# Kernel tuning notes

Hardware: AMD Instinct MI355X
Metric: run time of the kernel (lower is better)

## Reference

```python
import jax, jax.numpy as jnp
import numpy as np

B, I, D = 2048, 4096, 512          # batch of candidates, num rated items, item_dim
IE, UE = 512, 1024                 # item_emb, user_emb
D1, D2, D3 = 1024, 512, 256        # MLP dense widths


def setup_inputs() -> dict:
    key = jax.random.key(0)
    ks = jax.random.split(key, 16)
    s = 0.02  # weight init scale
    candidate_items = jax.random.normal(ks[0], (B, D), dtype=jnp.float32)
    rated_items = jax.random.normal(ks[1], (I, D), dtype=jnp.float32)
    ratings = jax.random.uniform(ks[2], (B, I), dtype=jnp.float32, minval=0.5, maxval=5.0)
    keep = jax.random.uniform(ks[3], (B, I)) < 0.05
    user_matrix = jnp.where(keep, ratings, 0.0)
    return dict(
        candidate_items=candidate_items,
        rated_items=rated_items,
        user_matrix=user_matrix,
        att_w=jax.random.normal(ks[4], (2 * D, 1), dtype=jnp.float32) * s,
        att_b=jnp.zeros((1,), jnp.float32),
        iw1=jax.random.normal(ks[5], (D, 2 * IE), dtype=jnp.float32) * s,
        ib1=jnp.zeros((2 * IE,), jnp.float32),
        iw2=jax.random.normal(ks[6], (2 * IE, IE), dtype=jnp.float32) * s,
        ib2=jnp.zeros((IE,), jnp.float32),
        uw1=jax.random.normal(ks[7], (D, 2 * UE), dtype=jnp.float32) * s,
        ub1=jnp.zeros((2 * UE,), jnp.float32),
        uw2=jax.random.normal(ks[8], (2 * UE, UE), dtype=jnp.float32) * s,
        ub2=jnp.zeros((UE,), jnp.float32),
        mw1=jax.random.normal(ks[9], (IE + UE, D1), dtype=jnp.float32) * s,
        mb1=jnp.zeros((D1,), jnp.float32),
        mw2=jax.random.normal(ks[10], (D1, D2), dtype=jnp.float32) * s,
        mb2=jnp.zeros((D2,), jnp.float32),
        mw3=jax.random.normal(ks[11], (D2, D3), dtype=jnp.float32) * s,
        mb3=jnp.zeros((D3,), jnp.float32),
        mw4=jax.random.normal(ks[12], (D3, 1), dtype=jnp.float32) * s,
        mb4=jnp.zeros((1,), jnp.float32),
    )


def reference(candidate_items, rated_items, user_matrix,
              att_w, att_b, iw1, ib1, iw2, ib2, uw1, ub1, uw2, ub2,
              mw1, mb1, mw2, mb2, mw3, mb3, mw4, mb4):
    d = candidate_items.shape[1]
    # AttentionNet(Linear(2D,1)) on cat(cand_repeat, rated_tile) decomposes exactly:
    # score[b,i] = cand[b] @ w_c + rated[i] @ w_r + b  (same math, no (B*I,2D) blowup)
    wc, wr = att_w[:d], att_w[d:]                      # (D,1), (D,1)
    scores = candidate_items @ wc + (rated_items @ wr).T + att_b  # (B, I)
    scores = jnp.where(user_matrix == 0.0, -jnp.inf, scores)
    att = jax.nn.softmax(scores, axis=1)
    att = jnp.nan_to_num(att, nan=0.0, posinf=0.0, neginf=0.0)  # rows with no ratings -> 0
    user_feat = (att * user_matrix) @ rated_items      # (B, D)
    # dual towers (dropout = identity in eval)
    item_emb = jax.nn.relu(jax.nn.relu(candidate_items @ iw1 + ib1) @ iw2 + ib2)
    user_emb = jax.nn.relu(jax.nn.relu(user_feat @ uw1 + ub1) @ uw2 + ub2)
    x = jnp.concatenate([item_emb, user_emb], axis=1)  # (B, IE+UE)
    x = jax.nn.relu(x @ mw1 + mb1)
    x = jax.nn.relu(x @ mw2 + mb2)
    x = jax.nn.relu(x @ mw3 + mb3)
    return x @ mw4 + mb4                               # (B, 1)
```

## Files before the change

### kernel.cpp

```cpp
#include <hip/hip_runtime.h>
#include <cstddef>

constexpr int Bn = 2048;
constexpr int In = 4096;
constexpr int Dn = 512;

typedef _Float16 f16;
typedef _Float16 f16x8 __attribute__((ext_vector_type(8)));
typedef _Float16 f16x4 __attribute__((ext_vector_type(4)));
typedef float    f32x4 __attribute__((ext_vector_type(4)));

__global__ __launch_bounds__(256) void k_rs(const float* __restrict__ rated,
                                            const float* __restrict__ att_w,
                                            float* __restrict__ rs) {
  const int wid  = threadIdx.x >> 6;
  const int lane = threadIdx.x & 63;
  const int i = blockIdx.x * 4 + wid;
  const float* row = rated + (size_t)i * Dn;
  const float* wr  = att_w + Dn;
  float s = 0.f;
  #pragma unroll
  for (int d = 0; d < Dn / 64; ++d)
    s = fmaf(row[lane + d * 64], wr[lane + d * 64], s);
  #pragma unroll
  for (int off = 32; off > 0; off >>= 1) s += __shfl_down(s, off);
  if (lane == 0) rs[i] = s;
}

__global__ __launch_bounds__(256) void k_userfeat(const float* __restrict__ um,
                                                  const float* __restrict__ rs,
                                                  const float* __restrict__ rated,
                                                  f16* __restrict__ uf) {
  __shared__ unsigned short s_idx[In];
  __shared__ float s_coef[In];
  __shared__ float s_red[8];
  __shared__ int s_cnt;
  const int tid = threadIdx.x;
  const int b = blockIdx.x;
  if (tid == 0) s_cnt = 0;
  __syncthreads();

  const float* umrow = um + (size_t)b * In;
  float lmax = -INFINITY;
  #pragma unroll
  for (int it = 0; it < In / 256; ++it) {
    const int i = tid + it * 256;
    const float u = umrow[i];
    if (u != 0.0f) {
      const int p = atomicAdd(&s_cnt, 1);
      s_idx[p] = (unsigned short)i;
      s_coef[p] = u;
      lmax = fmaxf(lmax, rs[i]);
    }
  }
  __syncthreads();
  const int n = s_cnt;

  #pragma unroll
  for (int off = 32; off > 0; off >>= 1) lmax = fmaxf(lmax, __shfl_down(lmax, off));
  if ((tid & 63) == 0) s_red[tid >> 6] = lmax;
  __syncthreads();
  const float m = fmaxf(fmaxf(s_red[0], s_red[1]), fmaxf(s_red[2], s_red[3]));
  __syncthreads();

  float lsum = 0.f;
  for (int j = tid; j < n; j += 256) {
    const float t = __expf(rs[s_idx[j]] - m);
    lsum += t;
    s_coef[j] = t * s_coef[j];
  }
  __syncthreads();
  #pragma unroll
  for (int off = 32; off > 0; off >>= 1) lsum += __shfl_down(lsum, off);
  if ((tid & 63) == 0) s_red[tid >> 6] = lsum;
  __syncthreads();
  const float S = s_red[0] + s_red[1] + s_red[2] + s_red[3];
  const float inv = (n > 0 && S > 0.f) ? 1.0f / S : 0.0f;

  float a0 = 0.f, a1 = 0.f;
  for (int j = 0; j < n; ++j) {
    const float c = s_coef[j];
    const float* rrow = rated + (size_t)s_idx[j] * Dn;
    a0 = fmaf(c, rrow[tid], a0);
    a1 = fmaf(c, rrow[tid + 256], a1);
  }
  uf[(size_t)b * Dn + tid]       = (f16)(a0 * inv);
  uf[(size_t)b * Dn + tid + 256] = (f16)(a1 * inv);
}

__global__ __launch_bounds__(256) void k_transpose_f2h(const float* __restrict__ src,
                                                       f16* __restrict__ dst,
                                                       int K, int N) {
  __shared__ float tile[32][33];
  const int tx = threadIdx.x & 31;
  const int ty = threadIdx.x >> 5;
  const int n0 = blockIdx.x * 32;
  const int k0 = blockIdx.y * 32;
  #pragma unroll
  for (int i = 0; i < 4; ++i)
    tile[ty + i * 8][tx] = src[(size_t)(k0 + ty + i * 8) * N + n0 + tx];
  __syncthreads();
  #pragma unroll
  for (int i = 0; i < 4; ++i)
    dst[(size_t)(n0 + ty + i * 8) * K + k0 + tx] = (f16)tile[tx][ty + i * 8];
}

__global__ __launch_bounds__(256) void k_cast_f2h(const float* __restrict__ src,
                                                  f16* __restrict__ dst, int n) {
  const int i = (blockIdx.x * 256 + threadIdx.x) * 4;
  if (i < n) {
    const float4 v = *reinterpret_cast<const float4*>(src + i);
    f16x4 h; h.x = (f16)v.x; h.y = (f16)v.y; h.z = (f16)v.z; h.w = (f16)v.w;
    *reinterpret_cast<f16x4*>(dst + i) = h;
  }
}

template <bool RELU>
__global__ __launch_bounds__(256) void k_hgemm(const f16* __restrict__ A,
                                               const f16* __restrict__ Wt,
                                               const float* __restrict__ bias,
                                               f16* __restrict__ C, int ldc,
                                               int N, int K) {
  __shared__ __align__(16) f16 As[64][40];
  __shared__ __align__(16) f16 Bs[64][40];

  const int tid  = threadIdx.x;
  const int lane = tid & 63;
  const int wave = tid >> 6;
  const int wr   = (wave >> 1) * 32;
  const int wc   = (wave & 1) * 32;
  const int lrow = lane & 15;
  const int koff = (lane >> 4) * 8;

  const int bm = blockIdx.y * 64;
  const int bn = blockIdx.x * 64;

  const int r   = tid >> 2;
  const int cof = (tid & 3) * 8;

  const f16* pa = A  + (size_t)(bm + r) * K + cof;
  const f16* pb = Wt + (size_t)(bn + r) * K + cof;

  f32x4 acc[2][2] = {};

  for (int k0 = 0; k0 < K; k0 += 32, pa += 32, pb += 32) {
    *reinterpret_cast<f16x8*>(&As[r][cof]) = *reinterpret_cast<const f16x8*>(pa);
    *reinterpret_cast<f16x8*>(&Bs[r][cof]) = *reinterpret_cast<const f16x8*>(pb);
    __syncthreads();

    const f16x8 a0 = *reinterpret_cast<const f16x8*>(&As[wr + lrow][koff]);
    const f16x8 a1 = *reinterpret_cast<const f16x8*>(&As[wr + 16 + lrow][koff]);
    const f16x8 b0 = *reinterpret_cast<const f16x8*>(&Bs[wc + lrow][koff]);
    const f16x8 b1 = *reinterpret_cast<const f16x8*>(&Bs[wc + 16 + lrow][koff]);

    acc[0][0] = __builtin_amdgcn_mfma_f32_16x16x32_f16(a0, b0, acc[0][0], 0, 0, 0);
    acc[0][1] = __builtin_amdgcn_mfma_f32_16x16x32_f16(a0, b1, acc[0][1], 0, 0, 0);
    acc[1][0] = __builtin_amdgcn_mfma_f32_16x16x32_f16(a1, b0, acc[1][0], 0, 0, 0);
    acc[1][1] = __builtin_amdgcn_mfma_f32_16x16x32_f16(a1, b1, acc[1][1], 0, 0, 0);
    __syncthreads();
  }

  const int orow = (lane >> 4) * 4;
  #pragma unroll
  for (int m = 0; m < 2; ++m)
    #pragma unroll
    for (int nn = 0; nn < 2; ++nn) {
      const int col = bn + wc + nn * 16 + lrow;
      const float bv = bias[col];
      #pragma unroll
      for (int rr = 0; rr < 4; ++rr) {
        const int row = bm + wr + m * 16 + orow + rr;
        float v = acc[m][nn][rr] + bv;
        if (RELU) v = fmaxf(v, 0.f);
        C[(size_t)row * ldc + col] = (f16)v;
      }
    }
}

__global__ __launch_bounds__(256) void k_final(const f16* __restrict__ h3,
                                               const float* __restrict__ mw4,
                                               const float* __restrict__ mb4,
                                               float* __restrict__ out) {
  const int wid = threadIdx.x >> 6;
  const int lane = threadIdx.x & 63;
  const int row = blockIdx.x * 4 + wid;
  const f16* hr = h3 + (size_t)row * 256;
  float s = 0.f;
  #pragma unroll
  for (int d = 0; d < 4; ++d)
    s = fmaf((float)hr[lane + d * 64], mw4[lane + d * 64], s);
  #pragma unroll
  for (int off = 32; off > 0; off >>= 1) s += __shfl_down(s, off);
  if (lane == 0) out[row] = s + mb4[0];
}

extern "C" void kernel_launch(void* const* d_in, const int* in_sizes, int n_in,
                              void* d_out, int out_size, void* d_ws, size_t ws_size,
                              hipStream_t stream) {
  const float* cand  = (const float*)d_in[0];
  const float* rated = (const float*)d_in[1];
  const float* um    = (const float*)d_in[2];
  const float* att_w = (const float*)d_in[3];
  const float* iw1 = (const float*)d_in[5];
  const float* ib1 = (const float*)d_in[6];
  const float* iw2 = (const float*)d_in[7];
  const float* ib2 = (const float*)d_in[8];
  const float* uw1 = (const float*)d_in[9];
  const float* ub1 = (const float*)d_in[10];
  const float* uw2 = (const float*)d_in[11];
  const float* ub2 = (const float*)d_in[12];
  const float* mw1 = (const float*)d_in[13];
  const float* mb1 = (const float*)d_in[14];
  const float* mw2 = (const float*)d_in[15];
  const float* mb2 = (const float*)d_in[16];
  const float* mw3 = (const float*)d_in[17];
  const float* mb3 = (const float*)d_in[18];
  const float* mw4 = (const float*)d_in[19];
  const float* mb4 = (const float*)d_in[20];
  float* out = (float*)d_out;

  f16*   hws = (f16*)d_ws;
  float* rs  = (float*)d_ws;
  size_t off = 8192;
  auto take = [&](size_t n) { f16* p = hws + off; off += n; return p; };
  f16* t_iw1 = take(512 * 1024);
  f16* t_iw2 = take(1024 * 512);
  f16* t_uw1 = take(512 * 2048);
  f16* t_uw2 = take(2048 * 1024);
  f16* t_mw1 = take(1536 * 1024);
  f16* t_mw2 = take(1024 * 512);
  f16* t_mw3 = take(512 * 256);
  f16* cand_h = take(2048 * 512);
  f16* uf_h   = take(2048 * 512);
  f16* Xc     = take(2048 * 1536);
  f16* big    = take(2048 * 2048);
  f16* h_i1 = big;
  f16* h_u1 = big;
  f16* h_m1 = big;
  f16* h_m2 = uf_h;
  f16* h_m3 = cand_h;

  dim3 blk(256);

  k_transpose_f2h<<<dim3(1024/32,  512/32), blk, 0, stream>>>(iw1, t_iw1,  512, 1024);
  k_transpose_f2h<<<dim3( 512/32, 1024/32), blk, 0, stream>>>(iw2, t_iw2, 1024,  512);
  k_transpose_f2h<<<dim3(2048/32,  512/32), blk, 0, stream>>>(uw1, t_uw1,  512, 2048);
  k_transpose_f2h<<<dim3(1024/32, 2048/32), blk, 0, stream>>>(uw2, t_uw2, 2048, 1024);
  k_transpose_f2h<<<dim3(1024/32, 1536/32), blk, 0, stream>>>(mw1, t_mw1, 1536, 1024);
  k_transpose_f2h<<<dim3( 512/32, 1024/32), blk, 0, stream>>>(mw2, t_mw2, 1024,  512);
  k_transpose_f2h<<<dim3( 256/32,  512/32), blk, 0, stream>>>(mw3, t_mw3,  512,  256);
  k_cast_f2h<<<dim3(Bn * Dn / 1024), blk, 0, stream>>>(cand, cand_h, Bn * Dn);

  k_rs<<<dim3(In / 4), blk, 0, stream>>>(rated, att_w, rs);

  k_userfeat<<<dim3(Bn), blk, 0, stream>>>(um, rs, rated, uf_h);

  k_hgemm<true><<<dim3(1024/64, Bn/64), blk, 0, stream>>>(cand_h, t_iw1, ib1, h_i1, 1024, 1024, 512);
  k_hgemm<true><<<dim3( 512/64, Bn/64), blk, 0, stream>>>(h_i1,   t_iw2, ib2, Xc,   1536,  512, 1024);

  k_hgemm<true><<<dim3(2048/64, Bn/64), blk, 0, stream>>>(uf_h, t_uw1, ub1, h_u1,     2048, 2048, 512);
  k_hgemm<true><<<dim3(1024/64, Bn/64), blk, 0, stream>>>(h_u1, t_uw2, ub2, Xc + 512, 1536, 1024, 2048);

  k_hgemm<true><<<dim3(1024/64, Bn/64), blk, 0, stream>>>(Xc,   t_mw1, mb1, h_m1, 1024, 1024, 1536);
  k_hgemm<true><<<dim3( 512/64, Bn/64), blk, 0, stream>>>(h_m1, t_mw2, mb2, h_m2,  512,  512, 1024);
  k_hgemm<true><<<dim3( 256/64, Bn/64), blk, 0, stream>>>(h_m2, t_mw3, mb3, h_m3,  256,  256, 512);

  k_final<<<dim3(Bn / 4), blk, 0, stream>>>(h_m3, mw4, mb4, out);
}
```

Before: 338.0 us.

## Replace sparse gather user-feature kernel with dense attention matrix plus MFMA GEMM

The per-row sparse gather-accumulate over rated items is replaced by a kernel that writes a dense fp16 attention-weight matrix (B x I), followed by a tensor-core GEMM against a transposed fp16 copy of rated_items. The shared HGEMM also moves to 128x64 tiles with K-step 64 and register prefetch of the next global tile, so loads overlap compute. This trades the scattered, uncoalesced row reads of the old kernel for dense MFMA work over a mostly-zero matrix, extra global traffic for the attention matrix, and an added transpose of rated_items. Precision drops to fp16 for the attention weights.

```diff
diff --git a/kernel.cpp b/kernel.cpp
--- a/kernel.cpp
+++ b/kernel.cpp
@@ -7,7 +7,6 @@
 
 typedef _Float16 f16;
 typedef _Float16 f16x8 __attribute__((ext_vector_type(8)));
-typedef _Float16 f16x4 __attribute__((ext_vector_type(4)));
 typedef float    f32x4 __attribute__((ext_vector_type(4)));
 
 __global__ __launch_bounds__(256) void k_rs(const float* __restrict__ rated,
@@ -27,65 +26,72 @@
   if (lane == 0) rs[i] = s;
 }
 
-__global__ __launch_bounds__(256) void k_userfeat(const float* __restrict__ um,
-                                                  const float* __restrict__ rs,
-                                                  const float* __restrict__ rated,
-                                                  f16* __restrict__ uf) {
-  __shared__ unsigned short s_idx[In];
-  __shared__ float s_coef[In];
-  __shared__ float s_red[8];
-  __shared__ int s_cnt;
+__global__ __launch_bounds__(256) void k_att(const float* __restrict__ um,
+                                             const float* __restrict__ rs,
+                                             f16* __restrict__ att) {
+  __shared__ float t[In];
+  __shared__ float red[4];
   const int tid = threadIdx.x;
   const int b = blockIdx.x;
-  if (tid == 0) s_cnt = 0;
+  const float* umrow = um + (size_t)b * In;
+
+  float ua[16];
+  float lmax = -INFINITY;
+  #pragma unroll
+  for (int it = 0; it < 4; ++it) {
+    const int i = (it * 256 + tid) * 4;
+    const float4 v = *reinterpret_cast<const float4*>(umrow + i);
+    ua[it * 4 + 0] = v.x; ua[it * 4 + 1] = v.y;
+    ua[it * 4 + 2] = v.z; ua[it * 4 + 3] = v.w;
+    #pragma unroll
+    for (int j = 0; j < 4; ++j) {
+      if (ua[it * 4 + j] != 0.f) {
+        const float r = rs[i + j];
+        t[i + j] = r;
+        lmax = fmaxf(lmax, r);
+      } else {
+        t[i + j] = -INFINITY;
+      }
+    }
+  }
+  #pragma unroll
+  for (int off = 32; off > 0; off >>= 1) lmax = fmaxf(lmax, __shfl_down(lmax, off));
+  if ((tid & 63) == 0) red[tid >> 6] = lmax;
   __syncthreads();
-
-  const float* umrow = um + (size_t)b * In;
-  float lmax = -INFINITY;
-  #pragma unroll
-  for (int it = 0; it < In / 256; ++it) {
-    const int i = tid + it * 256;
-    const float u = umrow[i];
-    if (u != 0.0f) {
-      const int p = atomicAdd(&s_cnt, 1);
-      s_idx[p] = (unsigned short)i;
-      s_coef[p] = u;
-      lmax = fmaxf(lmax, rs[i]);
-    }
-  }
+  const float m = fmaxf(fmaxf(red[0], red[1]), fmaxf(red[2], red[3]));
   __syncthreads();
-  const int n = s_cnt;
-
-  #pragma unroll
-  for (int off = 32; off > 0; off >>= 1) lmax = fmaxf(lmax, __shfl_down(lmax, off));
-  if ((tid & 63) == 0) s_red[tid >> 6] = lmax;
+
+  float lsum = 0.f;
+  #pragma unroll
+  for (int it = 0; it < 4; ++it) {
+    const int i = (it * 256 + tid) * 4;
+    #pragma unroll
+    for (int j = 0; j < 4; ++j) {
+      float v = 0.f;
+      if (ua[it * 4 + j] != 0.f) {
+        const float e = __expf(t[i + j] - m);
+        lsum += e;
+        v = e * ua[it * 4 + j];
+      }
+      t[i + j] = v;
+    }
+  }
+  #pragma unroll
+  for (int off = 32; off > 0; off >>= 1) lsum += __shfl_down(lsum, off);
+  if ((tid & 63) == 0) red[tid >> 6] = lsum;
   __syncthreads();
-  const float m = fmaxf(fmaxf(s_red[0], s_red[1]), fmaxf(s_red[2], s_red[3]));
-  __syncthreads();
-
-  float lsum = 0.f;
-  for (int j = tid; j < n; j += 256) {
-    const float t = __expf(rs[s_idx[j]] - m);
-    lsum += t;
-    s_coef[j] = t * s_coef[j];
-  }
-  __syncthreads();
-  #pragma unroll
-  for (int off = 32; off > 0; off >>= 1) lsum += __shfl_down(lsum, off);
-  if ((tid & 63) == 0) s_red[tid >> 6] = lsum;
-  __syncthreads();
-  const float S = s_red[0] + s_red[1] + s_red[2] + s_red[3];
-  const float inv = (n > 0 && S > 0.f) ? 1.0f / S : 0.0f;
-
-  float a0 = 0.f, a1 = 0.f;
-  for (int j = 0; j < n; ++j) {
-    const float c = s_coef[j];
-    const float* rrow = rated + (size_t)s_idx[j] * Dn;
-    a0 = fmaf(c, rrow[tid], a0);
-    a1 = fmaf(c, rrow[tid + 256], a1);
-  }
-  uf[(size_t)b * Dn + tid]       = (f16)(a0 * inv);
-  uf[(size_t)b * Dn + tid + 256] = (f16)(a1 * inv);
+  const float S = red[0] + red[1] + red[2] + red[3];
+  const float inv = (S > 0.f) ? 1.0f / S : 0.0f;
+
+  f16* arow = att + (size_t)b * In;
+  #pragma unroll
+  for (int it = 0; it < 2; ++it) {
+    const int i = (it * 256 + tid) * 8;
+    f16x8 h;
+    #pragma unroll
+    for (int j = 0; j < 8; ++j) h[j] = (f16)(t[i + j] * inv);
+    *reinterpret_cast<f16x8*>(arow + i) = h;
+  }
 }
 
 __global__ __launch_bounds__(256) void k_transpose_f2h(const float* __restrict__ src,
@@ -110,67 +116,100 @@
   const int i = (blockIdx.x * 256 + threadIdx.x) * 4;
   if (i < n) {
     const float4 v = *reinterpret_cast<const float4*>(src + i);
-    f16x4 h; h.x = (f16)v.x; h.y = (f16)v.y; h.z = (f16)v.z; h.w = (f16)v.w;
-    *reinterpret_cast<f16x4*>(dst + i) = h;
-  }
-}
-
-template <bool RELU>
+    f16 h0 = (f16)v.x, h1 = (f16)v.y, h2 = (f16)v.z, h3 = (f16)v.w;
+    f16* p = dst + i;
+    p[0] = h0; p[1] = h1; p[2] = h2; p[3] = h3;
+  }
+}
+
+template <bool RELU, bool BIAS>
 __global__ __launch_bounds__(256) void k_hgemm(const f16* __restrict__ A,
                                                const f16* __restrict__ Wt,
                                                const float* __restrict__ bias,
                                                f16* __restrict__ C, int ldc,
                                                int N, int K) {
-  __shared__ __align__(16) f16 As[64][40];
-  __shared__ __align__(16) f16 Bs[64][40];
+  __shared__ __align__(16) f16 As[128][72];
+  __shared__ __align__(16) f16 Bs[64][72];
 
   const int tid  = threadIdx.x;
   const int lane = tid & 63;
   const int wave = tid >> 6;
-  const int wr   = (wave >> 1) * 32;
-  const int wc   = (wave & 1) * 32;
+  const int wrow = (wave >> 1) * 64;
+  const int wcol = (wave & 1) * 32;
   const int lrow = lane & 15;
   const int koff = (lane >> 4) * 8;
 
-  const int bm = blockIdx.y * 64;
+  const int bm = blockIdx.y * 128;
   const int bn = blockIdx.x * 64;
 
-  const int r   = tid >> 2;
-  const int cof = (tid & 3) * 8;
-
-  const f16* pa = A  + (size_t)(bm + r) * K + cof;
-  const f16* pb = Wt + (size_t)(bn + r) * K + cof;
-
-  f32x4 acc[2][2] = {};
-
-  for (int k0 = 0; k0 < K; k0 += 32, pa += 32, pb += 32) {
-    *reinterpret_cast<f16x8*>(&As[r][cof]) = *reinterpret_cast<const f16x8*>(pa);
-    *reinterpret_cast<f16x8*>(&Bs[r][cof]) = *reinterpret_cast<const f16x8*>(pb);
+  const int ar = tid >> 1;
+  const int ac = (tid & 1) * 32;
+  const int br = tid >> 2;
+  const int bc = (tid & 3) * 16;
+
+  const f16* pa = A  + (size_t)(bm + ar) * K + ac;
+  const f16* pb = Wt + (size_t)(bn + br) * K + bc;
+
+  f16x8 ra0, ra1, ra2, ra3, rb0, rb1;
+  #define LOADG()                                                   \
+    ra0 = *reinterpret_cast<const f16x8*>(pa +  0);                 \
+    ra1 = *reinterpret_cast<const f16x8*>(pa +  8);                 \
+    ra2 = *reinterpret_cast<const f16x8*>(pa + 16);                 \
+    ra3 = *reinterpret_cast<const f16x8*>(pa + 24);                 \
+    rb0 = *reinterpret_cast<const f16x8*>(pb +  0);                 \
+    rb1 = *reinterpret_cast<const f16x8*>(pb +  8);
+
+  f32x4 acc[4][2] = {};
+
+  LOADG();
+  for (int k0 = 0; k0 < K; k0 += 64) {
+    *reinterpret_cast<f16x8*>(&As[ar][ac +  0]) = ra0;
+    *reinterpret_cast<f16x8*>(&As[ar][ac +  8]) = ra1;
+    *reinterpret_cast<f16x8*>(&As[ar][ac + 16]) = ra2;
+    *reinterpret_cast<f16x8*>(&As[ar][ac + 24]) = ra3;
+    *reinterpret_cast<f16x8*>(&Bs[br][bc +  0]) = rb0;
+    *reinterpret_cast<f16x8*>(&Bs[br][bc +  8]) = rb1;
     __syncthreads();
 
-    const f16x8 a0 = *reinterpret_cast<const f16x8*>(&As[wr + lrow][koff]);
-    const f16x8 a1 = *reinterpret_cast<const f16x8*>(&As[wr + 16 + lrow][koff]);
-    const f16x8 b0 = *reinterpret_cast<const f16x8*>(&Bs[wc + lrow][koff]);
-    const f16x8 b1 = *reinterpret_cast<const f16x8*>(&Bs[wc + 16 + lrow][koff]);
-
-    acc[0][0] = __builtin_amdgcn_mfma_f32_16x16x32_f16(a0, b0, acc[0][0], 0, 0, 0);
-    acc[0][1] = __builtin_amdgcn_mfma_f32_16x16x32_f16(a0, b1, acc[0][1], 0, 0, 0);
-    acc[1][0] = __builtin_amdgcn_mfma_f32_16x16x32_f16(a1, b0, acc[1][0], 0, 0, 0);
-    acc[1][1] = __builtin_amdgcn_mfma_f32_16x16x32_f16(a1, b1, acc[1][1], 0, 0, 0);
+    if (k0 + 64 < K) {
+      pa += 64; pb += 64;
+      LOADG();
+    }
+
+    #pragma unroll
+    for (int ks = 0; ks < 2; ++ks) {
+      const int kk = ks * 32 + koff;
+      const f16x8 a0 = *reinterpret_cast<const f16x8*>(&As[wrow +  0 + lrow][kk]);
+      const f16x8 a1 = *reinterpret_cast<const f16x8*>(&As[wrow + 16 + lrow][kk]);
+      const f16x8 a2 = *reinterpret_cast<const f16x8*>(&As[wrow + 32 + lrow][kk]);
+      const f16x8 a3 = *reinterpret_cast<const f16x8*>(&As[wrow + 48 + lrow][kk]);
+      const f16x8 b0 = *reinterpret_cast<const f16x8*>(&Bs[wcol +  0 + lrow][kk]);
+      const f16x8 b1 = *reinterpret_cast<const f16x8*>(&Bs[wcol + 16 + lrow][kk]);
+
+      acc[0][0] = __builtin_amdgcn_mfma_f32_16x16x32_f16(a0, b0, acc[0][0], 0, 0, 0);
+      acc[0][1] = __builtin_amdgcn_mfma_f32_16x16x32_f16(a0, b1, acc[0][1], 0, 0, 0);
+      acc[1][0] = __builtin_amdgcn_mfma_f32_16x16x32_f16(a1, b0, acc[1][0], 0, 0, 0);
+      acc[1][1] = __builtin_amdgcn_mfma_f32_16x16x32_f16(a1, b1, acc[1][1], 0, 0, 0);
+      acc[2][0] = __builtin_amdgcn_mfma_f32_16x16x32_f16(a2, b0, acc[2][0], 0, 0, 0);
+      acc[2][1] = __builtin_amdgcn_mfma_f32_16x16x32_f16(a2, b1, acc[2][1], 0, 0, 0);
+      acc[3][0] = __builtin_amdgcn_mfma_f32_16x16x32_f16(a3, b0, acc[3][0], 0, 0, 0);
+      acc[3][1] = __builtin_amdgcn_mfma_f32_16x16x32_f16(a3, b1, acc[3][1], 0, 0, 0);
+    }
     __syncthreads();
   }
+  #undef LOADG
 
   const int orow = (lane >> 4) * 4;
   #pragma unroll
-  for (int m = 0; m < 2; ++m)
-    #pragma unroll
-    for (int nn = 0; nn < 2; ++nn) {
-      const int col = bn + wc + nn * 16 + lrow;
-      const float bv = bias[col];
+  for (int mf = 0; mf < 4; ++mf)
+    #pragma unroll
+    for (int nf = 0; nf < 2; ++nf) {
+      const int col = bn + wcol + nf * 16 + lrow;
+      const float bv = BIAS ? bias[col] : 0.f;
       #pragma unroll
       for (int rr = 0; rr < 4; ++rr) {
-        const int row = bm + wr + m * 16 + orow + rr;
-        float v = acc[m][nn][rr] + bv;
+        const int row = bm + wrow + mf * 16 + orow + rr;
+        float v = acc[mf][nf][rr] + bv;
         if (RELU) v = fmaxf(v, 0.f);
         C[(size_t)row * ldc + col] = (f16)v;
       }
@@ -223,17 +262,21 @@
   float* rs  = (float*)d_ws;
   size_t off = 8192;
   auto take = [&](size_t n) { f16* p = hws + off; off += n; return p; };
-  f16* t_iw1 = take(512 * 1024);
-  f16* t_iw2 = take(1024 * 512);
-  f16* t_uw1 = take(512 * 2048);
-  f16* t_uw2 = take(2048 * 1024);
-  f16* t_mw1 = take(1536 * 1024);
-  f16* t_mw2 = take(1024 * 512);
-  f16* t_mw3 = take(512 * 256);
-  f16* cand_h = take(2048 * 512);
-  f16* uf_h   = take(2048 * 512);
-  f16* Xc     = take(2048 * 1536);
-  f16* big    = take(2048 * 2048);
+  f16* t_iw1   = take(512 * 1024);
+  f16* t_iw2   = take(1024 * 512);
+  f16* t_uw1   = take(512 * 2048);
+  f16* t_uw2   = take(2048 * 1024);
+  f16* t_mw1   = take(1536 * 1024);
+  f16* t_mw2   = take(1024 * 512);
+  f16* t_mw3   = take(512 * 256);
+  f16* t_rated = take(512 * 4096);
+  f16* cand_h  = take(2048 * 512);
+  f16* uf_h    = take(2048 * 512);
+  f16* big     = take(2048 * 2048);
+  f16* Xc      = take(2048 * 1536);
+  f16* spare   = take(2048 * 512);
+  (void)spare;
+  f16* att_d = big;
   f16* h_i1 = big;
   f16* h_u1 = big;
   f16* h_m1 = big;
@@ -242,6 +285,10 @@
 
   dim3 blk(256);
 
+  k_rs<<<dim3(In / 4), blk, 0, stream>>>(rated, att_w, rs);
+  k_att<<<dim3(Bn), blk, 0, stream>>>(um, rs, att_d);
+
+  k_transpose_f2h<<<dim3( 512/32, 4096/32), blk, 0, stream>>>(rated, t_rated, 4096, 512);
   k_transpose_f2h<<<dim3(1024/32,  512/32), blk, 0, stream>>>(iw1, t_iw1,  512, 1024);
   k_transpose_f2h<<<dim3( 512/32, 1024/32), blk, 0, stream>>>(iw2, t_iw2, 1024,  512);
   k_transpose_f2h<<<dim3(2048/32,  512/32), blk, 0, stream>>>(uw1, t_uw1,  512, 2048);
@@ -251,19 +298,18 @@
   k_transpose_f2h<<<dim3( 256/32,  512/32), blk, 0, stream>>>(mw3, t_mw3,  512,  256);
   k_cast_f2h<<<dim3(Bn * Dn / 1024), blk, 0, stream>>>(cand, cand_h, Bn * Dn);
 
-  k_rs<<<dim3(In / 4), blk, 0, stream>>>(rated, att_w, rs);
-
-  k_userfeat<<<dim3(Bn), blk, 0, stream>>>(um, rs, rated, uf_h);
-
-  k_hgemm<true><<<dim3(1024/64, Bn/64), blk, 0, stream>>>(cand_h, t_iw1, ib1, h_i1, 1024, 1024, 512);
-  k_hgemm<true><<<dim3( 512/64, Bn/64), blk, 0, stream>>>(h_i1,   t_iw2, ib2, Xc,   1536,  512, 1024);
-
-  k_hgemm<true><<<dim3(2048/64, Bn/64), blk, 0, stream>>>(uf_h, t_uw1, ub1, h_u1,     2048, 2048, 512);
-  k_hgemm<true><<<dim3(1024/64, Bn/64), blk, 0, stream>>>(h_u1, t_uw2, ub2, Xc + 512, 1536, 1024, 2048);
-
-  k_hgemm<true><<<dim3(1024/64, Bn/64), blk, 0, stream>>>(Xc,   t_mw1, mb1, h_m1, 1024, 1024, 1536);
-  k_hgemm<true><<<dim3( 512/64, Bn/64), blk, 0, stream>>>(h_m1, t_mw2, mb2, h_m2,  512,  512, 1024);
-  k_hgemm<true><<<dim3( 256/64, Bn/64), blk, 0, stream>>>(h_m2, t_mw3, mb3, h_m3,  256,  256, 512);
+  k_hgemm<false, false><<<dim3(512/64, Bn/128), blk, 0, stream>>>(
+      att_d, t_rated, nullptr, uf_h, 512, 512, 4096);
+
+  k_hgemm<true, true><<<dim3(1024/64, Bn/128), blk, 0, stream>>>(cand_h, t_iw1, ib1, h_i1, 1024, 1024, 512);
+  k_hgemm<true, true><<<dim3( 512/64, Bn/128), blk, 0, stream>>>(h_i1,   t_iw2, ib2, Xc,   1536,  512, 1024);
+
+  k_hgemm<true, true><<<dim3(2048/64, Bn/128), blk, 0, stream>>>(uf_h, t_uw1, ub1, h_u1,     2048, 2048, 512);
+  k_hgemm<true, true><<<dim3(1024/64, Bn/128), blk, 0, stream>>>(h_u1, t_uw2, ub2, Xc + 512, 1536, 1024, 2048);
+
+  k_hgemm<true, true><<<dim3(1024/64, Bn/128), blk, 0, stream>>>(Xc,   t_mw1, mb1, h_m1, 1024, 1024, 1536);
+  k_hgemm<true, true><<<dim3( 512/64, Bn/128), blk, 0, stream>>>(h_m1, t_mw2, mb2, h_m2,  512,  512, 1024);
+  k_hgemm<true, true><<<dim3( 256/64, Bn/128), blk, 0, stream>>>(h_m2, t_mw3, mb3, h_m3,  256,  256, 512);
 
   k_final<<<dim3(Bn / 4), blk, 0, stream>>>(h_m3, mw4, mb4, out);
 }
```

Result: faster. 320.5 us (-5.2%).
